# Performance work log

Measured on AMD Instinct MI355X. Metric: run time of the kernel, lower is better.

## Reference

```python
import jax, jax.numpy as jnp
import numpy as np
import math

EMB, HEAD, B, S = 1024, 64, 4, 4096

def setup_inputs() -> dict:
    key = jax.random.key(0)
    ks = jax.random.split(key, 7)
    scale = 1.0 / math.sqrt(EMB)
    return {
        "x": jax.random.normal(ks[0], (B, S, EMB), dtype=jnp.float32),
        "Wq": jax.random.uniform(ks[1], (EMB, HEAD), jnp.float32, -scale, scale),
        "bq": jax.random.uniform(ks[2], (HEAD,), jnp.float32, -scale, scale),
        "Wk": jax.random.uniform(ks[3], (EMB, HEAD), jnp.float32, -scale, scale),
        "bk": jax.random.uniform(ks[4], (HEAD,), jnp.float32, -scale, scale),
        "Wv": jax.random.uniform(ks[5], (EMB, HEAD), jnp.float32, -scale, scale),
        "bv": jax.random.uniform(ks[6], (HEAD,), jnp.float32, -scale, scale),
    }

def reference(x, Wq, bq, Wk, bk, Wv, bv):
    # x: [B, S, E]
    q = x @ Wq + bq            # [B, S, H]
    k = x @ Wk + bk
    v = x @ Wv + bv
    scores = jnp.einsum('bqh,bkh->bqk', q, k) / math.sqrt(q.shape[-1])
    # causal mask: position q attends to k <= q
    s = x.shape[1]
    causal = jnp.tril(jnp.ones((s, s), dtype=bool))
    scores = jnp.where(causal, scores, -jnp.inf)
    attn = jax.nn.softmax(scores, axis=-1)
    return jnp.einsum('bqk,bkh->bqh', attn, v)
```

## Files before the change

### kernel.cpp

```cpp
#include <hip/hip_runtime.h>
#include <hip/hip_bf16.h>
#include <math.h>

#define EMB 1024
#define HEAD 64
#define NB 4
#define SEQ 4096
#define MTOT (NB * SEQ)
#define QSCALE (0.125f * 1.44269504088896f)
#define MBOUND 4.0f

typedef __attribute__((ext_vector_type(8))) short bf16x8;
typedef __attribute__((ext_vector_type(4))) float f32x4;
typedef __attribute__((ext_vector_type(16))) float f32x16;
typedef __attribute__((ext_vector_type(2))) unsigned u32x2;

static __device__ __forceinline__ unsigned short f2b(float f) {
    union { float f; unsigned u; } v; v.f = f;
    unsigned r = v.u + 0x7FFFu + ((v.u >> 16) & 1u);
    return (unsigned short)(r >> 16);
}
static __device__ __forceinline__ float b2f(unsigned short u) {
    union { unsigned u; float f; } v; v.u = ((unsigned)u) << 16; return v.f;
}
static __device__ __forceinline__ unsigned pk2(float lo, float hi) {
    unsigned r;
    asm("v_cvt_pk_bf16_f32 %0, %1, %2" : "=v"(r) : "v"(lo), "v"(hi));
    return r;
}
static __device__ __forceinline__ float ex2(float x) {
    float r;
    asm("v_exp_f32 %0, %1" : "=v"(r) : "v"(x));
    return r;
}

__global__ void wb_kernel(const float* __restrict__ Wq, const float* __restrict__ Wk,
                          const float* __restrict__ Wv, unsigned short* __restrict__ Wb) {
    const int f = blockIdx.x % 12, ks = blockIdx.x / 12;
    const int t = threadIdx.x;
    const int h = t >> 7, lane = (t >> 1) & 63, j0 = (t & 1) * 4;
    const int li = lane & 15, lg = lane >> 4;
    const float* W = (f < 4) ? Wq : (f < 8) ? Wk : Wv;
    const int nc = (f & 3) * 16 + li;
    const int k0 = ks * 64 + h * 32 + lg * 8 + j0;
    const unsigned u0 = pk2(W[(size_t)(k0 + 0) * HEAD + nc], W[(size_t)(k0 + 1) * HEAD + nc]);
    const unsigned u1 = pk2(W[(size_t)(k0 + 2) * HEAD + nc], W[(size_t)(k0 + 3) * HEAD + nc]);
    unsigned short* dst = Wb + (size_t)(f * 16 + ks) * 1024 + h * 512 + lane * 8 + j0;
    *(u32x2*)dst = (u32x2){u0, u1};
}

__global__ __launch_bounds__(256) void proj_kernel(
    const float* __restrict__ x, const unsigned short* __restrict__ Wb,
    const float* __restrict__ bq, const float* __restrict__ bk,
    const float* __restrict__ bv, unsigned short* __restrict__ qb,
    unsigned short* __restrict__ kb, unsigned short* __restrict__ vb) {
    __shared__ unsigned short Xl[32][1032];

    const int tid = threadIdx.x;
    const int wave = tid >> 6, lane = tid & 63;
    const int li = lane & 15, lg = lane >> 4;
    const int mh = wave & 1, nh = wave >> 1;
    const int rbase = blockIdx.x * 32;

    {
        const int row = tid >> 3, c8 = tid & 7;
        const float* xr = x + (size_t)(rbase + row) * EMB;
#pragma unroll
        for (int j = 0; j < 16; ++j) {
            const int col = j * 64 + c8 * 8;
            const float4 t0 = *(const float4*)(xr + col);
            const float4 t1 = *(const float4*)(xr + col + 4);
            union { bf16x8 v; unsigned u[4]; } pa;
            pa.u[0] = pk2(t0.x, t0.y); pa.u[1] = pk2(t0.z, t0.w);
            pa.u[2] = pk2(t1.x, t1.y); pa.u[3] = pk2(t1.z, t1.w);
            *(bf16x8*)&Xl[row][col] = pa.v;
        }
    }
    __syncthreads();

    f32x4 acc[6];
#pragma unroll
    for (int n = 0; n < 6; ++n) acc[n] = (f32x4){0.f, 0.f, 0.f, 0.f};

    for (int ks = 0; ks < 16; ++ks) {
        const bf16x8 a0 = *(const bf16x8*)&Xl[mh * 16 + li][ks * 64 + lg * 8];
        const bf16x8 a1 = *(const bf16x8*)&Xl[mh * 16 + li][ks * 64 + 32 + lg * 8];
#pragma unroll
        for (int n = 0; n < 6; ++n) {
            const int f = nh * 6 + n;
            const unsigned short* wp = Wb + (size_t)(f * 16 + ks) * 1024 + lane * 8;
            const bf16x8 b0 = *(const bf16x8*)(wp);
            const bf16x8 b1 = *(const bf16x8*)(wp + 512);
            if (f < 8) {
                acc[n] = __builtin_amdgcn_mfma_f32_16x16x32_bf16(b0, a0, acc[n], 0, 0, 0);
                acc[n] = __builtin_amdgcn_mfma_f32_16x16x32_bf16(b1, a1, acc[n], 0, 0, 0);
            } else {
                acc[n] = __builtin_amdgcn_mfma_f32_16x16x32_bf16(a0, b0, acc[n], 0, 0, 0);
                acc[n] = __builtin_amdgcn_mfma_f32_16x16x32_bf16(a1, b1, acc[n], 0, 0, 0);
            }
        }
    }

    const int si0 = rbase & 4095, bi = rbase >> 12;
#pragma unroll
    for (int n = 0; n < 6; ++n) {
        const int f = nh * 6 + n;
        if (f < 8) {
            const float* bias = (f < 4) ? bq : bk;
            const int dbase = (f & 3) * 16 + lg * 4;
            const float4 bb = *(const float4*)&bias[dbase];
            const float qs = (f < 4) ? QSCALE : 1.0f;
            unsigned short* dst = (f < 4) ? qb : kb;
            const size_t plane = (size_t)((bi * 2 + (lg >> 1)) * 4 + (f & 3)) * (SEQ * 8);
            const unsigned u0 = pk2((acc[n][0] + bb.x) * qs, (acc[n][1] + bb.y) * qs);
            const unsigned u1 = pk2((acc[n][2] + bb.z) * qs, (acc[n][3] + bb.w) * qs);
            unsigned short* p = dst + plane + (size_t)(si0 + mh * 16 + li) * 8 + (lg & 1) * 4;
            *(u32x2*)p = (u32x2){u0, u1};
        } else {
            const int nc = (f & 3) * 16 + li;
            const float bb = bv[nc];
            const unsigned u0 = pk2(acc[n][0] + bb, acc[n][1] + bb);
            const unsigned u1 = pk2(acc[n][2] + bb, acc[n][3] + bb);
            const int si = si0 + mh * 16 + lg * 4;
            unsigned short* p = vb + ((size_t)bi * 512 + (si >> 3)) * 512 + nc * 8 + (si & 7);
            *(u32x2*)p = (u32x2){u0, u1};
        }
    }
}

template<int W64, int NWIN, int KMAX>
__global__ __launch_bounds__(256) void attn_kernel(
    const unsigned short* __restrict__ Qb, const unsigned short* __restrict__ Kb,
    const unsigned short* __restrict__ Vb, unsigned* __restrict__ pO,
    float* __restrict__ pL) {
    const int lane = threadIdx.x & 63;
    const int ql = lane & 31, h = lane >> 5;
    const int b = blockIdx.y;
    const int w = blockIdx.x * 4 + (threadIdx.x >> 6);
    int seg = 0;
#pragma unroll
    for (int kk = 1; kk < KMAX; ++kk)
        if (w >= 128 * kk - W64 * kk * (kk - 1)) seg = kk;
    const int Os = 128 * seg - W64 * seg * (seg - 1);
    const int qidx = 2 * W64 * seg + (w - Os);
    const int tdiag = qidx >> 1;
    const int qa0 = qidx * 32;
    const int t0 = W64 * seg;
    const int tend = (t0 + W64 < tdiag + 1) ? t0 + W64 : tdiag + 1;

    const unsigned short* qb0 = Qb + ((size_t)(b * 2 + h)) * 4 * (SEQ * 8);
    const unsigned short* kb0 = Kb + ((size_t)(b * 2 + h)) * 4 * (SEQ * 8);
    const unsigned short* vb0 = Vb + (size_t)b * 512 * 512;

    bf16x8 qf[4];
#pragma unroll
    for (int s = 0; s < 4; ++s)
        qf[s] = *(const bf16x8*)(qb0 + (size_t)s * (SEQ * 8) + (size_t)(qa0 + ql) * 8);

    f32x16 oa0, oa1;
#pragma unroll
    for (int r = 0; r < 16; ++r) { oa0[r] = 0.f; oa1[r] = 0.f; }
    float lsum = 0.f;

    bf16x8 kcur[2][4], knxt[2][4];
#pragma unroll
    for (int hh = 0; hh < 2; ++hh)
#pragma unroll
        for (int s = 0; s < 4; ++s)
            kcur[hh][s] = *(const bf16x8*)(kb0 + (size_t)s * (SEQ * 8)
                                           + ((size_t)t0 * 64 + 32 * hh + ql) * 8);

    for (int t = t0; t < tend; ++t) {
        bf16x8 vf[2][4];
#pragma unroll
        for (int dt = 0; dt < 2; ++dt)
#pragma unroll
            for (int cc = 0; cc < 4; ++cc)
                vf[dt][cc] = *(const bf16x8*)(vb0 + ((size_t)t * 8 + 2 * cc + h) * 512
                                              + (dt * 32 + ql) * 8);

        f32x16 st0, st1;
#pragma unroll
        for (int r = 0; r < 16; ++r) { st0[r] = 0.f; st1[r] = 0.f; }
        __builtin_amdgcn_s_setprio(1);
#pragma unroll
        for (int s = 0; s < 4; ++s) {
            st0 = __builtin_amdgcn_mfma_f32_32x32x16_bf16(kcur[0][s], qf[s], st0, 0, 0, 0);
            st1 = __builtin_amdgcn_mfma_f32_32x32x16_bf16(kcur[1][s], qf[s], st1, 0, 0, 0);
        }
        __builtin_amdgcn_s_setprio(0);

        if (t + 1 < tend) {
#pragma unroll
            for (int hh = 0; hh < 2; ++hh)
#pragma unroll
                for (int s = 0; s < 4; ++s)
                    knxt[hh][s] = *(const bf16x8*)(kb0 + (size_t)s * (SEQ * 8)
                                                   + ((size_t)(t + 1) * 64 + 32 * hh + ql) * 8);
        }

        if (t == tdiag) {
            if (qidx & 1) {
#pragma unroll
                for (int r = 0; r < 16; ++r) {
                    const int kvl = (r & 3) + 8 * (r >> 2) + 4 * h;
                    if (kvl > ql) st1[r] = -1e30f;
                }
            } else {
#pragma unroll
                for (int r = 0; r < 16; ++r) {
                    const int kvl = (r & 3) + 8 * (r >> 2) + 4 * h;
                    if (kvl > ql) st0[r] = -1e30f;
                    st1[r] = -1e30f;
                }
            }
        }
#pragma unroll
        for (int r = 0; r < 16; ++r) {
            st0[r] = ex2(st0[r] - MBOUND);
            st1[r] = ex2(st1[r] - MBOUND);
        }
        {
            float q0 = (st0[0] + st0[1]) + (st0[2] + st0[3]);
            float q1 = (st0[4] + st0[5]) + (st0[6] + st0[7]);
            float q2 = (st0[8] + st0[9]) + (st0[10] + st0[11]);
            float q3 = (st0[12] + st0[13]) + (st0[14] + st0[15]);
            float q4 = (st1[0] + st1[1]) + (st1[2] + st1[3]);
            float q5 = (st1[4] + st1[5]) + (st1[6] + st1[7]);
            float q6 = (st1[8] + st1[9]) + (st1[10] + st1[11]);
            float q7 = (st1[12] + st1[13]) + (st1[14] + st1[15]);
            lsum += ((q0 + q1) + (q2 + q3)) + ((q4 + q5) + (q6 + q7));
        }

        bf16x8 bfv[4];
#pragma unroll
        for (int hh = 0; hh < 2; ++hh) {
            unsigned w8[8];
#pragma unroll
            for (int tt = 0; tt < 8; ++tt)
                w8[tt] = hh ? pk2(st1[2 * tt], st1[2 * tt + 1])
                            : pk2(st0[2 * tt], st0[2 * tt + 1]);
            const unsigned xa0 = h ? w8[0] : w8[2];
            const unsigned va0 = __shfl_xor((int)xa0, 32);
            const unsigned xb0 = h ? w8[1] : w8[3];
            const unsigned vb_0 = __shfl_xor((int)xb0, 32);
            union { bf16x8 v; unsigned u[4]; } bbv;
            bbv.u[0] = h ? va0 : w8[0];
            bbv.u[1] = h ? vb_0 : w8[1];
            bbv.u[2] = h ? w8[2] : va0;
            bbv.u[3] = h ? w8[3] : vb_0;
            bfv[hh * 2] = bbv.v;
            const unsigned xa1 = h ? w8[4] : w8[6];
            const unsigned va1 = __shfl_xor((int)xa1, 32);
            const unsigned xb1 = h ? w8[5] : w8[7];
            const unsigned vb_1 = __shfl_xor((int)xb1, 32);
            bbv.u[0] = h ? va1 : w8[4];
            bbv.u[1] = h ? vb_1 : w8[5];
            bbv.u[2] = h ? w8[6] : va1;
            bbv.u[3] = h ? w8[7] : vb_1;
            bfv[hh * 2 + 1] = bbv.v;
        }
        __builtin_amdgcn_s_setprio(1);
#pragma unroll
        for (int cc = 0; cc < 4; ++cc) {
            oa0 = __builtin_amdgcn_mfma_f32_32x32x16_bf16(vf[0][cc], bfv[cc], oa0, 0, 0, 0);
            oa1 = __builtin_amdgcn_mfma_f32_32x32x16_bf16(vf[1][cc], bfv[cc], oa1, 0, 0, 0);
        }
        __builtin_amdgcn_s_setprio(0);

#pragma unroll
        for (int hh = 0; hh < 2; ++hh)
#pragma unroll
            for (int s = 0; s < 4; ++s)
                kcur[hh][s] = knxt[hh][s];
    }

    lsum += __shfl_xor(lsum, 32);
    const size_t gw = (size_t)b * NWIN + w;
    unsigned* po = pO + gw * 1024;
#pragma unroll
    for (int r = 0; r < 16; r += 2) {
        const int dp = ((r & 3) >> 1) + 4 * (r >> 2) + 2 * h;
        po[dp * 32 + ql] = pk2(oa0[r], oa0[r + 1]);
        po[(16 + dp) * 32 + ql] = pk2(oa1[r], oa1[r + 1]);
    }
    if (h == 0) pL[gw * 32 + ql] = lsum;
}

template<int W64, int NWIN>
__global__ __launch_bounds__(256) void merge_kernel(
    const unsigned* __restrict__ pO, const float* __restrict__ pL,
    float* __restrict__ out) {
    const int qidx = blockIdx.x, b = blockIdx.y;
    const int wcount = qidx / (2 * W64) + 1;
    const int t = threadIdx.x;
    const int ql = t & 31, g = t >> 5;

    float acc[8] = {0.f, 0.f, 0.f, 0.f, 0.f, 0.f, 0.f, 0.f};
    float L = 0.f;
    for (int k = 0; k < wcount; ++k) {
        const int Os = 128 * k - W64 * k * (k - 1);
        const size_t gw = (size_t)b * NWIN + Os + (qidx - 2 * W64 * k);
        L += pL[gw * 32 + ql];
#pragma unroll
        for (int i = 0; i < 4; ++i) {
            const unsigned u = pO[gw * 1024 + (size_t)(g * 4 + i) * 32 + ql];
            acc[2 * i] += b2f((unsigned short)(u & 0xFFFFu));
            acc[2 * i + 1] += b2f((unsigned short)(u >> 16));
        }
    }
    const float inv = 1.0f / L;
    float* op = out + ((size_t)b * SEQ + qidx * 32 + ql) * HEAD + g * 8;
    f32x4 o0 = {acc[0] * inv, acc[1] * inv, acc[2] * inv, acc[3] * inv};
    f32x4 o1 = {acc[4] * inv, acc[5] * inv, acc[6] * inv, acc[7] * inv};
    *(f32x4*)(op) = o0;
    *(f32x4*)(op + 4) = o1;
}

extern "C" void kernel_launch(void* const* d_in, const int* in_sizes, int n_in,
                              void* d_out, int out_size, void* d_ws, size_t ws_size,
                              hipStream_t stream) {
    const float* x  = (const float*)d_in[0];
    const float* Wq = (const float*)d_in[1];
    const float* bq = (const float*)d_in[2];
    const float* Wk = (const float*)d_in[3];
    const float* bk = (const float*)d_in[4];
    const float* Wv = (const float*)d_in[5];
    const float* bv = (const float*)d_in[6];

    unsigned short* Wb = (unsigned short*)d_ws;
    unsigned short* qb = Wb + 3 * HEAD * EMB;
    unsigned short* kb = qb + (size_t)MTOT * HEAD;
    unsigned short* vb = kb + (size_t)MTOT * HEAD;
    unsigned* pO = (unsigned*)(vb + (size_t)MTOT * HEAD);
    const size_t base_shorts = (size_t)3 * HEAD * EMB + (size_t)3 * MTOT * HEAD;

    wb_kernel<<<dim3(192), dim3(256), 0, stream>>>(Wq, Wk, Wv, Wb);
    proj_kernel<<<dim3(MTOT / 32), dim3(256), 0, stream>>>(x, Wb, bq, bk, bv, qb, kb, vb);

    const size_t need4 = base_shorts * 2 + (size_t)NB * 1088 * (1024 * 4 + 32 * 4);
    if (ws_size >= need4) {
        float* pL = (float*)(pO + (size_t)NB * 1088 * 1024);
        attn_kernel<4, 1088, 16><<<dim3(272, NB), dim3(256), 0, stream>>>(qb, kb, vb, pO, pL);
        merge_kernel<4, 1088><<<dim3(128, NB), dim3(256), 0, stream>>>(pO, pL, (float*)d_out);
    } else {
        float* pL = (float*)(pO + (size_t)NB * 576 * 1024);
        attn_kernel<8, 576, 8><<<dim3(144, NB), dim3(256), 0, stream>>>(qb, kb, vb, pO, pL);
        merge_kernel<8, 576><<<dim3(128, NB), dim3(256), 0, stream>>>(pO, pL, (float*)d_out);
    }
}
```

Before: 75.24 us.

## Shrink projection tiles to 16 rows and double-buffer weight fragment loads

The projection kernel now processes 16 rows per block instead of 32, so the grid doubles and LDS use halves. Each wave now owns 3 of the 12 output feature tiles instead of 6. The global loads of the next k-step's weight fragments are software-pipelined into alternating register buffers, so load latency overlaps the MFMAs of the current step. The cost is twice as much total weight traffic from L2 (each block rereads all of Wb for half as many rows) and higher register pressure from the fully unrolled k loop.

```diff
diff --git a/kernel.cpp b/kernel.cpp
--- a/kernel.cpp
+++ b/kernel.cpp
@@ -54,20 +54,19 @@
     const float* __restrict__ bq, const float* __restrict__ bk,
     const float* __restrict__ bv, unsigned short* __restrict__ qb,
     unsigned short* __restrict__ kb, unsigned short* __restrict__ vb) {
-    __shared__ unsigned short Xl[32][1032];
+    __shared__ unsigned short Xl[16][1032];
 
     const int tid = threadIdx.x;
-    const int wave = tid >> 6, lane = tid & 63;
+    const int nh = tid >> 6, lane = tid & 63;
     const int li = lane & 15, lg = lane >> 4;
-    const int mh = wave & 1, nh = wave >> 1;
-    const int rbase = blockIdx.x * 32;
+    const int rbase = blockIdx.x * 16;
 
     {
-        const int row = tid >> 3, c8 = tid & 7;
+        const int row = tid >> 4, cf = (tid & 15) * 8;
         const float* xr = x + (size_t)(rbase + row) * EMB;
 #pragma unroll
-        for (int j = 0; j < 16; ++j) {
-            const int col = j * 64 + c8 * 8;
+        for (int j = 0; j < 8; ++j) {
+            const int col = j * 128 + cf;
             const float4 t0 = *(const float4*)(xr + col);
             const float4 t1 = *(const float4*)(xr + col + 4);
             union { bf16x8 v; unsigned u[4]; } pa;
@@ -78,19 +77,34 @@
     }
     __syncthreads();
 
-    f32x4 acc[6];
-#pragma unroll
-    for (int n = 0; n < 6; ++n) acc[n] = (f32x4){0.f, 0.f, 0.f, 0.f};
-
+    f32x4 acc[3];
+#pragma unroll
+    for (int n = 0; n < 3; ++n) acc[n] = (f32x4){0.f, 0.f, 0.f, 0.f};
+
+    bf16x8 wA[3][2], wB[3][2];
+#pragma unroll
+    for (int n = 0; n < 3; ++n) {
+        const unsigned short* wp = Wb + (size_t)((nh * 3 + n) * 16 + 0) * 1024 + lane * 8;
+        wA[n][0] = *(const bf16x8*)(wp);
+        wA[n][1] = *(const bf16x8*)(wp + 512);
+    }
+#pragma unroll
     for (int ks = 0; ks < 16; ++ks) {
-        const bf16x8 a0 = *(const bf16x8*)&Xl[mh * 16 + li][ks * 64 + lg * 8];
-        const bf16x8 a1 = *(const bf16x8*)&Xl[mh * 16 + li][ks * 64 + 32 + lg * 8];
-#pragma unroll
-        for (int n = 0; n < 6; ++n) {
-            const int f = nh * 6 + n;
-            const unsigned short* wp = Wb + (size_t)(f * 16 + ks) * 1024 + lane * 8;
-            const bf16x8 b0 = *(const bf16x8*)(wp);
-            const bf16x8 b1 = *(const bf16x8*)(wp + 512);
+        if (ks < 15) {
+#pragma unroll
+            for (int n = 0; n < 3; ++n) {
+                const unsigned short* wp = Wb + (size_t)((nh * 3 + n) * 16 + ks + 1) * 1024 + lane * 8;
+                if (ks & 1) { wA[n][0] = *(const bf16x8*)(wp); wA[n][1] = *(const bf16x8*)(wp + 512); }
+                else        { wB[n][0] = *(const bf16x8*)(wp); wB[n][1] = *(const bf16x8*)(wp + 512); }
+            }
+        }
+        const bf16x8 a0 = *(const bf16x8*)&Xl[li][ks * 64 + lg * 8];
+        const bf16x8 a1 = *(const bf16x8*)&Xl[li][ks * 64 + 32 + lg * 8];
+#pragma unroll
+        for (int n = 0; n < 3; ++n) {
+            const int f = nh * 3 + n;
+            const bf16x8 b0 = (ks & 1) ? wB[n][0] : wA[n][0];
+            const bf16x8 b1 = (ks & 1) ? wB[n][1] : wA[n][1];
             if (f < 8) {
                 acc[n] = __builtin_amdgcn_mfma_f32_16x16x32_bf16(b0, a0, acc[n], 0, 0, 0);
                 acc[n] = __builtin_amdgcn_mfma_f32_16x16x32_bf16(b1, a1, acc[n], 0, 0, 0);
@@ -103,8 +117,8 @@
 
     const int si0 = rbase & 4095, bi = rbase >> 12;
 #pragma unroll
-    for (int n = 0; n < 6; ++n) {
-        const int f = nh * 6 + n;
+    for (int n = 0; n < 3; ++n) {
+        const int f = nh * 3 + n;
         if (f < 8) {
             const float* bias = (f < 4) ? bq : bk;
             const int dbase = (f & 3) * 16 + lg * 4;
@@ -114,14 +128,14 @@
             const size_t plane = (size_t)((bi * 2 + (lg >> 1)) * 4 + (f & 3)) * (SEQ * 8);
             const unsigned u0 = pk2((acc[n][0] + bb.x) * qs, (acc[n][1] + bb.y) * qs);
             const unsigned u1 = pk2((acc[n][2] + bb.z) * qs, (acc[n][3] + bb.w) * qs);
-            unsigned short* p = dst + plane + (size_t)(si0 + mh * 16 + li) * 8 + (lg & 1) * 4;
+            unsigned short* p = dst + plane + (size_t)(si0 + li) * 8 + (lg & 1) * 4;
             *(u32x2*)p = (u32x2){u0, u1};
         } else {
             const int nc = (f & 3) * 16 + li;
             const float bb = bv[nc];
             const unsigned u0 = pk2(acc[n][0] + bb, acc[n][1] + bb);
             const unsigned u1 = pk2(acc[n][2] + bb, acc[n][3] + bb);
-            const int si = si0 + mh * 16 + lg * 4;
+            const int si = si0 + lg * 4;
             unsigned short* p = vb + ((size_t)bi * 512 + (si >> 3)) * 512 + nc * 8 + (si & 7);
             *(u32x2*)p = (u32x2){u0, u1};
         }
@@ -336,7 +350,7 @@
     const size_t base_shorts = (size_t)3 * HEAD * EMB + (size_t)3 * MTOT * HEAD;
 
     wb_kernel<<<dim3(192), dim3(256), 0, stream>>>(Wq, Wk, Wv, Wb);
-    proj_kernel<<<dim3(MTOT / 32), dim3(256), 0, stream>>>(x, Wb, bq, bk, bv, qb, kb, vb);
+    proj_kernel<<<dim3(MTOT / 16), dim3(256), 0, stream>>>(x, Wb, bq, bk, bv, qb, kb, vb);
 
     const size_t need4 = base_shorts * 2 + (size_t)NB * 1088 * (1024 * 4 + 32 * 4);
     if (ws_size >= need4) {
```

After: 62.87 us. 1.2x faster.
